# Performance work log

Measured on AMD Instinct MI355X. Metric: run time of the kernel, lower is better.

Reference implementation:

```python
import jax, jax.numpy as jnp
import numpy as np

D_IN = 2048
NUM_HEADS = 16
QK_NOPE = 64
QK_ROPE = 64
QK_HEAD = QK_NOPE + QK_ROPE  # 128
V_HEAD = 128
KV_LORA = 1024
SEQ = 4096
BATCH = 1
SCALE = QK_HEAD ** -0.5
EPS = 1e-6


def rmsnorm(x, w):
    return x * jax.lax.rsqrt(jnp.mean(x * x, axis=-1, keepdims=True) + EPS) * w


def apply_rope(x, cos, sin):
    # x: [B, S, H, D]; cos/sin: [S, D//2]; pairs are consecutive elements (view_as_complex)
    b, s, h, d = x.shape
    xr = x.reshape(b, s, h, d // 2, 2)
    xe, xo = xr[..., 0], xr[..., 1]
    c = cos[None, :, None, :]
    sn = sin[None, :, None, :]
    oe = xe * c - xo * sn
    oo = xe * sn + xo * c
    return jnp.stack([oe, oo], axis=-1).reshape(b, s, h, d)


def setup_inputs() -> dict:
    key = jax.random.key(0)
    ks = jax.random.split(key, 8)
    x = jax.random.normal(ks[0], (BATCH, SEQ, D_IN), dtype=jnp.float32)
    # rotary tables (rope_theta=10000)
    inv_freq = 1.0 / (10000.0 ** (np.arange(0, QK_ROPE, 2, dtype=np.float32) / QK_ROPE))
    angles = np.arange(SEQ, dtype=np.float32)[:, None] * inv_freq[None, :]
    cos = jnp.asarray(np.cos(angles), dtype=jnp.float32)
    sin = jnp.asarray(np.sin(angles), dtype=jnp.float32)
    # causal additive mask [S, S]
    mask = jnp.where(jnp.triu(jnp.ones((SEQ, SEQ), dtype=bool), k=1), -1e9, 0.0).astype(jnp.float32)
    def lin(k, fan_out, fan_in):
        bound = 1.0 / np.sqrt(fan_in)
        return jax.random.uniform(k, (fan_out, fan_in), jnp.float32, -bound, bound)
    wq = lin(ks[1], NUM_HEADS * QK_HEAD, D_IN)
    wkv_a = lin(ks[2], KV_LORA + QK_ROPE, D_IN)
    kv_norm_w = jnp.ones((KV_LORA,), dtype=jnp.float32)
    wkv_b = lin(ks[3], NUM_HEADS * (QK_NOPE + V_HEAD), KV_LORA)
    wo = lin(ks[4], D_IN, NUM_HEADS * V_HEAD)
    return {"x": x, "cos": cos, "sin": sin, "mask": mask, "wq": wq,
            "wkv_a": wkv_a, "kv_norm_w": kv_norm_w, "wkv_b": wkv_b, "wo": wo,
            "start_pos": 0}


def reference(x, cos, sin, mask, wq, wkv_a, kv_norm_w, wkv_b, wo, start_pos):
    b, s, _ = x.shape
    # Q projection -> [B, S, H, qk_head_dim]
    q = (x @ wq.T).reshape(b, s, NUM_HEADS, QK_HEAD)
    q_nope, q_pe = q[..., :QK_NOPE], q[..., QK_NOPE:]
    q_pe = apply_rope(q_pe, cos, sin)
    # KV low-rank projection
    kv_full = x @ wkv_a.T                               # [B, S, KV_LORA + QK_ROPE]
    kv, k_pe = kv_full[..., :KV_LORA], kv_full[..., KV_LORA:]
    k_pe = apply_rope(k_pe[:, :, None, :], cos, sin)    # [B, S, 1, QK_ROPE]
    # naive path: expand latent to per-head k_nope / v
    q = jnp.concatenate([q_nope, q_pe], axis=-1)        # [B, S, H, 128]
    kvb = (rmsnorm(kv, kv_norm_w) @ wkv_b.T).reshape(b, s, NUM_HEADS, QK_NOPE + V_HEAD)
    k_nope, v = kvb[..., :QK_NOPE], kvb[..., QK_NOPE:]
    k = jnp.concatenate([k_nope, jnp.broadcast_to(k_pe, (b, s, NUM_HEADS, QK_ROPE))], axis=-1)
    # start_pos=0 prefill: cache[:, :end_pos] == freshly written k, v
    scores = jnp.einsum('bqhd,bkhd->bqhk', q, k) * SCALE  # [B, S, H, S]
    scores = scores + mask[None, :, None, :]
    probs = jax.nn.softmax(scores.astype(jnp.float32), axis=-1).astype(x.dtype)
    out = jnp.einsum('bqhk,bkhd->bqhd', probs, v)       # [B, S, H, V_HEAD]
    return out.reshape(b, s, NUM_HEADS * V_HEAD) @ wo.T
```

## Files before the change

kernel.cpp:

```cpp
#include <hip/hip_runtime.h>

typedef __bf16 bf16;
typedef __attribute__((ext_vector_type(8))) __bf16 bf16x8;
typedef __attribute__((ext_vector_type(2))) __bf16 bf16x2;
typedef __attribute__((ext_vector_type(4))) float f32x4;
typedef __attribute__((ext_vector_type(4))) int int4v;

typedef __attribute__((address_space(1))) const void gconst_t;
typedef __attribute__((address_space(3))) void lvoid_t;

#define SEQ 4096
#define D_IN 2048
#define NHEADS 16
#define QSCALE (0.08838834764831843f * 1.4426950408889634f)
#define RMS_EPS 1e-6f

__device__ inline unsigned pack2bf(float a, float b) {
    bf16x2 t; t[0] = (bf16)a; t[1] = (bf16)b;
    return __builtin_bit_cast(unsigned, t);
}

__global__ __launch_bounds__(256) void f32_to_bf16_kernel(
    const float* __restrict__ in, bf16* __restrict__ out, int n) {
    int i = (blockIdx.x * 256 + threadIdx.x) * 4;
    int stride = gridDim.x * 256 * 4;
    for (; i < n; i += stride) {
        float4 v = *reinterpret_cast<const float4*>(in + i);
        bf16 o[4];
        o[0] = (bf16)v.x; o[1] = (bf16)v.y; o[2] = (bf16)v.z; o[3] = (bf16)v.w;
        *reinterpret_cast<uint2*>(out + i) = *reinterpret_cast<uint2*>(o);
    }
}

template<bool BF16_OUT>
__global__ __launch_bounds__(256) void gemm_bt_kernel(
    const bf16* __restrict__ A, const bf16* __restrict__ B, void* __restrict__ Cout,
    int M, int N, int K) {
    __shared__ __align__(16) bf16 Al[128 * 32];
    __shared__ __align__(16) bf16 Bl[128 * 32];
    int tid  = threadIdx.x;
    int lane = tid & 63;
    int w    = tid >> 6;
    int wr = w >> 1, wc = w & 1;
    int m0 = blockIdx.y * 128;
    int n0 = blockIdx.x * 128;
    int l15 = lane & 15;
    int g   = lane >> 4;

    int srow = (lane >> 2);
    int scol = (lane & 3) * 8;

    f32x4 acc[4][4] = {};

    for (int k0 = 0; k0 < K; k0 += 32) {
        __syncthreads();
        #pragma unroll
        for (int c = 0; c < 2; c++) {
            int arow = m0 + c*64 + w*16 + srow;
            const bf16* ga = A + (size_t)arow * K + k0 + scol;
            __builtin_amdgcn_global_load_lds((gconst_t*)ga, (lvoid_t*)&Al[c*2048 + w*512], 16, 0, 0);
            int brow = n0 + c*64 + w*16 + srow; if (brow >= N) brow = N - 1;
            const bf16* gb = B + (size_t)brow * K + k0 + scol;
            __builtin_amdgcn_global_load_lds((gconst_t*)gb, (lvoid_t*)&Bl[c*2048 + w*512], 16, 0, 0);
        }
        __syncthreads();
        bf16x8 af[4], bfv[4];
        #pragma unroll
        for (int mt = 0; mt < 4; mt++)
            af[mt] = *reinterpret_cast<const bf16x8*>(&Al[(wr*64 + mt*16 + l15) * 32 + g*8]);
        #pragma unroll
        for (int nt = 0; nt < 4; nt++)
            bfv[nt] = *reinterpret_cast<const bf16x8*>(&Bl[(wc*64 + nt*16 + l15) * 32 + g*8]);
        #pragma unroll
        for (int mt = 0; mt < 4; mt++)
            #pragma unroll
            for (int nt = 0; nt < 4; nt++)
                acc[mt][nt] = __builtin_amdgcn_mfma_f32_16x16x32_bf16(af[mt], bfv[nt], acc[mt][nt], 0, 0, 0);
    }

    #pragma unroll
    for (int mt = 0; mt < 4; mt++) {
        #pragma unroll
        for (int nt = 0; nt < 4; nt++) {
            int col = n0 + wc*64 + nt*16 + l15;
            if (col < N) {
                #pragma unroll
                for (int r = 0; r < 4; r++) {
                    int row = m0 + wr*64 + mt*16 + g*4 + r;
                    if (BF16_OUT)
                        ((bf16*)Cout)[(size_t)row * N + col] = (bf16)acc[mt][nt][r];
                    else
                        ((float*)Cout)[(size_t)row * N + col] = acc[mt][nt][r];
                }
            }
        }
    }
}

__global__ __launch_bounds__(256) void prep_q_kernel(
    bf16* __restrict__ q, const float* __restrict__ cosb, const float* __restrict__ sinb) {
    int s = blockIdx.x;
    int t = threadIdx.x;
    bf16* p = q + (size_t)s * 2048 + t * 8;
    bf16x8 v = *reinterpret_cast<bf16x8*>(p);
    float f[8];
    #pragma unroll
    for (int j = 0; j < 8; j++) f[j] = (float)v[j];
    int d0 = (t & 15) * 8;
    if (d0 >= 64) {
        int ib = (d0 - 64) >> 1;
        #pragma unroll
        for (int pr = 0; pr < 4; pr++) {
            float c  = cosb[s * 32 + ib + pr];
            float sn = sinb[s * 32 + ib + pr];
            float xe = f[pr*2], xo = f[pr*2 + 1];
            f[pr*2]     = xe * c - xo * sn;
            f[pr*2 + 1] = xe * sn + xo * c;
        }
    }
    #pragma unroll
    for (int j = 0; j < 8; j++) v[j] = (bf16)(f[j] * QSCALE);
    *reinterpret_cast<bf16x8*>(p) = v;
}

__global__ __launch_bounds__(256) void prep_kv_kernel(
    const bf16* __restrict__ kvfull, const float* __restrict__ w,
    const float* __restrict__ cosb, const float* __restrict__ sinb,
    bf16* __restrict__ kvnorm, bf16* __restrict__ kpe) {
    __shared__ float red[4];
    int s = blockIdx.x;
    int t = threadIdx.x;
    const bf16* src = kvfull + (size_t)s * 1088;
    float f[4];
    {
        uint2 raw = *reinterpret_cast<const uint2*>(src + t * 4);
        bf16* vb = reinterpret_cast<bf16*>(&raw);
        float ss = 0.f;
        #pragma unroll
        for (int j = 0; j < 4; j++) { f[j] = (float)vb[j]; ss += f[j] * f[j]; }
        #pragma unroll
        for (int m = 1; m < 64; m <<= 1) ss += __shfl_xor(ss, m);
        if ((t & 63) == 0) red[t >> 6] = ss;
    }
    __syncthreads();
    float tot = red[0] + red[1] + red[2] + red[3];
    float rms = rsqrtf(tot * (1.0f / 1024.0f) + RMS_EPS);
    bf16 o[4];
    #pragma unroll
    for (int j = 0; j < 4; j++) o[j] = (bf16)(f[j] * rms * w[t*4 + j]);
    *reinterpret_cast<uint2*>(kvnorm + (size_t)s * 1024 + t * 4) = *reinterpret_cast<uint2*>(o);
    if (t < 16) {
        float e[4];
        #pragma unroll
        for (int j = 0; j < 4; j++) e[j] = (float)src[1024 + t*4 + j];
        int ib = t * 2;
        float c0 = cosb[s*32 + ib],     s0 = sinb[s*32 + ib];
        float c1 = cosb[s*32 + ib + 1], s1 = sinb[s*32 + ib + 1];
        bf16 ko[4];
        ko[0] = (bf16)(e[0]*c0 - e[1]*s0);
        ko[1] = (bf16)(e[0]*s0 + e[1]*c0);
        ko[2] = (bf16)(e[2]*c1 - e[3]*s1);
        ko[3] = (bf16)(e[2]*s1 + e[3]*c1);
        *reinterpret_cast<uint2*>(kpe + (size_t)s * 64 + t * 4) = *reinterpret_cast<uint2*>(ko);
    }
}

__global__ __launch_bounds__(256) void build_vt_kernel(
    const bf16* __restrict__ kvb, bf16* __restrict__ vt) {
    const int LT = 130;
    __shared__ bf16 lt[64 * 130];
    int h  = blockIdx.y;
    int s0 = blockIdx.x * 64;
    int t  = threadIdx.x;
    {
        int row = t >> 2;
        int d0  = (t & 3) * 32;
        const bf16* src = kvb + (size_t)(s0 + row) * 3072 + h * 192 + 64 + d0;
        int4v v0 = *reinterpret_cast<const int4v*>(src);
        int4v v1 = *reinterpret_cast<const int4v*>(src + 8);
        int4v v2 = *reinterpret_cast<const int4v*>(src + 16);
        int4v v3 = *reinterpret_cast<const int4v*>(src + 24);
        int* dst = reinterpret_cast<int*>(&lt[row * LT + d0]);
        int* s0p = reinterpret_cast<int*>(&v0); int* s1p = reinterpret_cast<int*>(&v1);
        int* s2p = reinterpret_cast<int*>(&v2); int* s3p = reinterpret_cast<int*>(&v3);
        #pragma unroll
        for (int j = 0; j < 4; j++) { dst[j] = s0p[j]; dst[4+j] = s1p[j]; dst[8+j] = s2p[j]; dst[12+j] = s3p[j]; }
    }
    __syncthreads();
    int ss = t & 63;
    int db = t >> 6;
    bf16* out = vt + (size_t)h * 128 * 4096 + s0 + ss;
    #pragma unroll
    for (int dd = db; dd < 128; dd += 4)
        out[(size_t)dd * 4096] = lt[ss * LT + dd];
}

__global__ __launch_bounds__(256, 2) void attn_kernel(
    const bf16* __restrict__ q,
    const bf16* __restrict__ kvb,
    const bf16* __restrict__ kpe,
    const bf16* __restrict__ vt,
    bf16* __restrict__ attn) {
    const int LPS = 72;
    __shared__ __align__(16) bf16 Kl[2][64 * 128];
    __shared__ __align__(16) bf16 Vl[2][128 * 64];
    __shared__ __align__(16) bf16 Pl[4][16 * 72];
    __shared__ __align__(16) float bcast[4][16];

    int h    = blockIdx.y;
    int tile = (h < 8) ? (31 - (int)blockIdx.x) : (int)blockIdx.x;
    int q0   = tile * 128;
    int t  = threadIdx.x;
    int lane = t & 63;
    int w  = t >> 6;
    int l15 = lane & 15;
    int g   = lane >> 4;
    int sw  = l15 & 7;
    int qrow = q0 + w * 32;

    const bf16* kvbh = kvb + h * 192;
    const bf16* vth  = vt + (size_t)h * 524288;

    bf16x8 qf[2][4];
    #pragma unroll
    for (int mt = 0; mt < 2; mt++) {
        const bf16* qp = q + (size_t)(qrow + mt*16 + l15) * 2048 + h * 128 + g * 8;
        #pragma unroll
        for (int c = 0; c < 4; c++) qf[mt][c] = *reinterpret_cast<const bf16x8*>(qp + c * 32);
    }

    f32x4 o[2][8] = {};
    float mrow[2], lrow[2];
    #pragma unroll
    for (int mt = 0; mt < 2; mt++) { mrow[mt] = -3e38f; lrow[mt] = 0.f; }

    int nch = (q0 >> 6) + 2;
    int dc  = (q0 >> 6) + (w >> 1);

    auto stageK = [&](int jc, int buf) {
        int j0 = jc << 6;
        #pragma unroll
        for (int c = 0; c < 4; c++) {
            int idx = c*256 + w*64 + lane;
            int row = idx >> 4;
            int u   = (idx & 15) ^ (row & 7);
            const bf16* src = (u < 8)
                ? kvbh + (size_t)(j0 + row) * 3072 + u * 8
                : kpe  + (size_t)(j0 + row) * 64  + (u - 8) * 8;
            __builtin_amdgcn_global_load_lds((gconst_t*)src,
                (lvoid_t*)&Kl[buf][(c*256 + w*64) * 8], 16, 0, 0);
        }
    };
    auto stageV = [&](int jc, int buf) {
        int j0 = jc << 6;
        #pragma unroll
        for (int c = 0; c < 4; c++) {
            int idx = c*256 + w*64 + lane;
            int row = idx >> 3;
            int u   = (idx & 7) ^ (row & 7);
            const bf16* src = vth + (size_t)row * 4096 + j0 + u * 8;
            __builtin_amdgcn_global_load_lds((gconst_t*)src,
                (lvoid_t*)&Vl[buf][(c*256 + w*64) * 8], 16, 0, 0);
        }
    };

    stageK(0, 0); stageV(0, 0);

    for (int jc = 0; jc < nch; ++jc) {
        __syncthreads();
        if (jc + 1 < nch) { stageK(jc + 1, (jc + 1) & 1); stageV(jc + 1, (jc + 1) & 1); }

        if (jc <= dc) {
            int cur = jc & 1;
            int j0  = jc << 6;
            bool masked = (jc == dc);

            f32x4 sfr[2][4];
            #pragma unroll
            for (int s = 0; s < 4; ++s) {
                int krow = s*16 + l15;
                bf16x8 kf[4];
                #pragma unroll
                for (int c = 0; c < 4; ++c)
                    kf[c] = *reinterpret_cast<const bf16x8*>(
                        &Kl[cur][krow*128 + (((c*4 + g) ^ sw) * 8)]);
                #pragma unroll
                for (int mt = 0; mt < 2; ++mt) {
                    f32x4 acc = {};
                    acc = __builtin_amdgcn_mfma_f32_16x16x32_bf16(kf[0], qf[mt][0], acc, 0, 0, 0);
                    acc = __builtin_amdgcn_mfma_f32_16x16x32_bf16(kf[1], qf[mt][1], acc, 0, 0, 0);
                    acc = __builtin_amdgcn_mfma_f32_16x16x32_bf16(kf[2], qf[mt][2], acc, 0, 0, 0);
                    acc = __builtin_amdgcn_mfma_f32_16x16x32_bf16(kf[3], qf[mt][3], acc, 0, 0, 0);
                    sfr[mt][s] = acc;
                }
            }

            bf16x8 pf[2][2];
            #pragma unroll
            for (int mt = 0; mt < 2; ++mt) {
                int i = qrow + mt*16 + l15;
                if (masked) {
                    #pragma unroll
                    for (int s = 0; s < 4; ++s)
                        #pragma unroll
                        for (int r = 0; r < 4; ++r) {
                            int j = j0 + s*16 + g*4 + r;
                            if (j > i) sfr[mt][s][r] = -3e38f;
                        }
                }
                float m01 = fmaxf(fmaxf(sfr[mt][0][0], sfr[mt][0][1]),
                                  fmaxf(sfr[mt][0][2], sfr[mt][0][3]));
                float m23 = fmaxf(fmaxf(sfr[mt][1][0], sfr[mt][1][1]),
                                  fmaxf(sfr[mt][1][2], sfr[mt][1][3]));
                float m45 = fmaxf(fmaxf(sfr[mt][2][0], sfr[mt][2][1]),
                                  fmaxf(sfr[mt][2][2], sfr[mt][2][3]));
                float m67 = fmaxf(fmaxf(sfr[mt][3][0], sfr[mt][3][1]),
                                  fmaxf(sfr[mt][3][2], sfr[mt][3][3]));
                float mloc = fmaxf(fmaxf(m01, m23), fmaxf(m45, m67));
                float mx = fmaxf(mloc, __shfl_xor(mloc, 16));
                mx = fmaxf(mx, __shfl_xor(mx, 32));
                bool need = mx > mrow[mt];
                float mnew = fmaxf(mrow[mt], mx);
                float sfac = __builtin_amdgcn_exp2f(mrow[mt] - mnew);
                mrow[mt] = mnew;
                float psum = 0.f;
                #pragma unroll
                for (int s = 0; s < 4; ++s)
                    #pragma unroll
                    for (int r = 0; r < 4; ++r) {
                        float p = __builtin_amdgcn_exp2f(sfr[mt][s][r] - mnew);
                        sfr[mt][s][r] = p;
                        psum += p;
                    }
                lrow[mt] = lrow[mt] * sfac + psum;
                #pragma unroll
                for (int s = 0; s < 4; ++s) {
                    unsigned u0 = pack2bf(sfr[mt][s][0], sfr[mt][s][1]);
                    unsigned u1 = pack2bf(sfr[mt][s][2], sfr[mt][s][3]);
                    *reinterpret_cast<unsigned*>(&Pl[w][l15 * LPS + s*16 + g*4])     = u0;
                    *reinterpret_cast<unsigned*>(&Pl[w][l15 * LPS + s*16 + g*4 + 2]) = u1;
                }
                if (g == 0) bcast[w][l15] = sfac;
                f32x4 sf4 = *reinterpret_cast<const f32x4*>(&bcast[w][g*4]);
                if (__any(need)) {
                    #pragma unroll
                    for (int dt = 0; dt < 8; ++dt)
                        #pragma unroll
                        for (int r = 0; r < 4; ++r) o[mt][dt][r] *= sf4[r];
                }
                pf[mt][0] = *reinterpret_cast<const bf16x8*>(&Pl[w][l15 * LPS + g * 8]);
                pf[mt][1] = *reinterpret_cast<const bf16x8*>(&Pl[w][l15 * LPS + 32 + g * 8]);
            }

            #pragma unroll
            for (int dt = 0; dt < 8; ++dt) {
                int vrow = dt*16 + l15;
                bf16x8 va = *reinterpret_cast<const bf16x8*>(
                    &Vl[cur][vrow*64 + ((g ^ sw) * 8)]);
                bf16x8 vb = *reinterpret_cast<const bf16x8*>(
                    &Vl[cur][vrow*64 + (((4 + g) ^ sw) * 8)]);
                o[0][dt] = __builtin_amdgcn_mfma_f32_16x16x32_bf16(pf[0][0], va, o[0][dt], 0, 0, 0);
                o[0][dt] = __builtin_amdgcn_mfma_f32_16x16x32_bf16(pf[0][1], vb, o[0][dt], 0, 0, 0);
                o[1][dt] = __builtin_amdgcn_mfma_f32_16x16x32_bf16(pf[1][0], va, o[1][dt], 0, 0, 0);
                o[1][dt] = __builtin_amdgcn_mfma_f32_16x16x32_bf16(pf[1][1], vb, o[1][dt], 0, 0, 0);
            }
        }
    }

    #pragma unroll
    for (int mt = 0; mt < 2; ++mt) {
        float l = lrow[mt];
        l += __shfl_xor(l, 16);
        l += __shfl_xor(l, 32);
        float linv = __builtin_amdgcn_rcpf(l);
        if (g == 0) bcast[w][l15] = linv;
        f32x4 li4 = *reinterpret_cast<const f32x4*>(&bcast[w][g*4]);
        #pragma unroll
        for (int r = 0; r < 4; ++r) {
            int i = qrow + mt*16 + g*4 + r;
            #pragma unroll
            for (int dt = 0; dt < 8; ++dt)
                attn[(size_t)i * 2048 + h * 128 + dt*16 + l15] = (bf16)(o[mt][dt][r] * li4[r]);
        }
    }
}

extern "C" void kernel_launch(void* const* d_in, const int* in_sizes, int n_in,
                              void* d_out, int out_size, void* d_ws, size_t ws_size,
                              hipStream_t stream) {
    const float* x    = (const float*)d_in[0];
    const float* cosb = (const float*)d_in[1];
    const float* sinb = (const float*)d_in[2];
    const float* wq   = (const float*)d_in[4];
    const float* wkva = (const float*)d_in[5];
    const float* kvw  = (const float*)d_in[6];
    const float* wkvb = (const float*)d_in[7];
    const float* wo   = (const float*)d_in[8];

    char* ws = (char*)d_ws;
    bf16* x_bf    = (bf16*)(ws + 0);
    bf16* kvnorm  = (bf16*)(ws + 0);
    bf16* attn    = (bf16*)(ws + 0);
    bf16* wq_bf   = (bf16*)(ws + 16777216);
    bf16* wkva_bf = (bf16*)(ws + 25165824);
    bf16* wkvb_bf = (bf16*)(ws + 29622272);
    bf16* wo_bf   = (bf16*)(ws + 35913728);
    bf16* q_bf    = (bf16*)(ws + 44302336);
    bf16* kvfull  = (bf16*)(ws + 61079552);
    bf16* kpe     = (bf16*)(ws + 69992448);
    bf16* kvb     = (bf16*)(ws + 70516736);
    bf16* vt      = (bf16*)(ws + 95682560);

    f32_to_bf16_kernel<<<dim3(512), dim3(256), 0, stream>>>(x,    x_bf,    4096*2048);
    f32_to_bf16_kernel<<<dim3(512), dim3(256), 0, stream>>>(wq,   wq_bf,   2048*2048);
    f32_to_bf16_kernel<<<dim3(512), dim3(256), 0, stream>>>(wkva, wkva_bf, 1088*2048);
    f32_to_bf16_kernel<<<dim3(512), dim3(256), 0, stream>>>(wkvb, wkvb_bf, 3072*1024);
    f32_to_bf16_kernel<<<dim3(512), dim3(256), 0, stream>>>(wo,   wo_bf,   2048*2048);

    gemm_bt_kernel<true><<<dim3(16, 32), dim3(256), 0, stream>>>(x_bf, wq_bf,   q_bf,   4096, 2048, 2048);
    gemm_bt_kernel<true><<<dim3(9,  32), dim3(256), 0, stream>>>(x_bf, wkva_bf, kvfull, 4096, 1088, 2048);

    prep_q_kernel <<<dim3(4096), dim3(256), 0, stream>>>(q_bf, cosb, sinb);
    prep_kv_kernel<<<dim3(4096), dim3(256), 0, stream>>>(kvfull, kvw, cosb, sinb, kvnorm, kpe);

    gemm_bt_kernel<true><<<dim3(24, 32), dim3(256), 0, stream>>>(kvnorm, wkvb_bf, kvb, 4096, 3072, 1024);

    build_vt_kernel<<<dim3(64, 16), dim3(256), 0, stream>>>(kvb, vt);

    attn_kernel<<<dim3(32, 16), dim3(256), 0, stream>>>(q_bf, kvb, kpe, vt, attn);

    gemm_bt_kernel<false><<<dim3(16, 32), dim3(256), 0, stream>>>(attn, wo_bf, (float*)d_out, 4096, 2048, 2048);
}
```

Measured before the change: 382.7 us.

## Fuse Q and KV-A projections into one GEMM, merge conversions, raise MFMA priority

The Q and KV-A weight buffers sit back to back in the workspace, so one GEMM with N=3136 now writes a combined qkv buffer. The prep kernels and attention read Q and KV from that buffer with the new row stride. The five fp32-to-bf16 conversion launches are merged into one kernel. s_setprio is raised around the QK and PV MFMA loops in attention. The aim is to cut launch overhead and GEMM tail waste, in exchange for a strided Q layout in the attention loads.

```diff
diff --git a/kernel.cpp b/kernel.cpp
--- a/kernel.cpp
+++ b/kernel.cpp
@@ -14,22 +14,36 @@
 #define NHEADS 16
 #define QSCALE (0.08838834764831843f * 1.4426950408889634f)
 #define RMS_EPS 1e-6f
+#define QKV_N 3136
 
 __device__ inline unsigned pack2bf(float a, float b) {
     bf16x2 t; t[0] = (bf16)a; t[1] = (bf16)b;
     return __builtin_bit_cast(unsigned, t);
 }
 
-__global__ __launch_bounds__(256) void f32_to_bf16_kernel(
-    const float* __restrict__ in, bf16* __restrict__ out, int n) {
-    int i = (blockIdx.x * 256 + threadIdx.x) * 4;
-    int stride = gridDim.x * 256 * 4;
-    for (; i < n; i += stride) {
+__device__ inline void conv_seg(const float* __restrict__ in, bf16* __restrict__ out,
+                                int n, int i0, int stride) {
+    for (int i = i0; i < n; i += stride) {
         float4 v = *reinterpret_cast<const float4*>(in + i);
         bf16 o[4];
         o[0] = (bf16)v.x; o[1] = (bf16)v.y; o[2] = (bf16)v.z; o[3] = (bf16)v.w;
         *reinterpret_cast<uint2*>(out + i) = *reinterpret_cast<uint2*>(o);
     }
+}
+
+__global__ __launch_bounds__(256) void convert_all_kernel(
+    const float* __restrict__ xs,  const float* __restrict__ wqs,
+    const float* __restrict__ was, const float* __restrict__ wbs,
+    const float* __restrict__ wos,
+    bf16* __restrict__ xd, bf16* __restrict__ wqd, bf16* __restrict__ wad,
+    bf16* __restrict__ wbd, bf16* __restrict__ wod) {
+    int i0 = (blockIdx.x * 256 + threadIdx.x) * 4;
+    int stride = gridDim.x * 256 * 4;
+    conv_seg(xs,  xd,  4096 * 2048, i0, stride);
+    conv_seg(wqs, wqd, 2048 * 2048, i0, stride);
+    conv_seg(was, wad, 1088 * 2048, i0, stride);
+    conv_seg(wbs, wbd, 3072 * 1024, i0, stride);
+    conv_seg(wos, wod, 2048 * 2048, i0, stride);
 }
 
 template<bool BF16_OUT>
@@ -98,10 +112,10 @@
 }
 
 __global__ __launch_bounds__(256) void prep_q_kernel(
-    bf16* __restrict__ q, const float* __restrict__ cosb, const float* __restrict__ sinb) {
+    bf16* __restrict__ qkv, const float* __restrict__ cosb, const float* __restrict__ sinb) {
     int s = blockIdx.x;
     int t = threadIdx.x;
-    bf16* p = q + (size_t)s * 2048 + t * 8;
+    bf16* p = qkv + (size_t)s * QKV_N + t * 8;
     bf16x8 v = *reinterpret_cast<bf16x8*>(p);
     float f[8];
     #pragma unroll
@@ -124,13 +138,13 @@
 }
 
 __global__ __launch_bounds__(256) void prep_kv_kernel(
-    const bf16* __restrict__ kvfull, const float* __restrict__ w,
+    const bf16* __restrict__ qkv, const float* __restrict__ w,
     const float* __restrict__ cosb, const float* __restrict__ sinb,
     bf16* __restrict__ kvnorm, bf16* __restrict__ kpe) {
     __shared__ float red[4];
     int s = blockIdx.x;
     int t = threadIdx.x;
-    const bf16* src = kvfull + (size_t)s * 1088;
+    const bf16* src = qkv + (size_t)s * QKV_N + 2048;
     float f[4];
     {
         uint2 raw = *reinterpret_cast<const uint2*>(src + t * 4);
@@ -224,7 +238,7 @@
     bf16x8 qf[2][4];
     #pragma unroll
     for (int mt = 0; mt < 2; mt++) {
-        const bf16* qp = q + (size_t)(qrow + mt*16 + l15) * 2048 + h * 128 + g * 8;
+        const bf16* qp = q + (size_t)(qrow + mt*16 + l15) * QKV_N + h * 128 + g * 8;
         #pragma unroll
         for (int c = 0; c < 4; c++) qf[mt][c] = *reinterpret_cast<const bf16x8*>(qp + c * 32);
     }
@@ -276,6 +290,7 @@
             bool masked = (jc == dc);
 
             f32x4 sfr[2][4];
+            __builtin_amdgcn_s_setprio(1);
             #pragma unroll
             for (int s = 0; s < 4; ++s) {
                 int krow = s*16 + l15;
@@ -294,6 +309,7 @@
                     sfr[mt][s] = acc;
                 }
             }
+            __builtin_amdgcn_s_setprio(0);
 
             bf16x8 pf[2][2];
             #pragma unroll
@@ -352,6 +368,7 @@
                 pf[mt][1] = *reinterpret_cast<const bf16x8*>(&Pl[w][l15 * LPS + 32 + g * 8]);
             }
 
+            __builtin_amdgcn_s_setprio(1);
             #pragma unroll
             for (int dt = 0; dt < 8; ++dt) {
                 int vrow = dt*16 + l15;
@@ -364,6 +381,7 @@
                 o[1][dt] = __builtin_amdgcn_mfma_f32_16x16x32_bf16(pf[1][0], va, o[1][dt], 0, 0, 0);
                 o[1][dt] = __builtin_amdgcn_mfma_f32_16x16x32_bf16(pf[1][1], vb, o[1][dt], 0, 0, 0);
             }
+            __builtin_amdgcn_s_setprio(0);
         }
     }
 
@@ -405,29 +423,24 @@
     bf16* wkva_bf = (bf16*)(ws + 25165824);
     bf16* wkvb_bf = (bf16*)(ws + 29622272);
     bf16* wo_bf   = (bf16*)(ws + 35913728);
-    bf16* q_bf    = (bf16*)(ws + 44302336);
-    bf16* kvfull  = (bf16*)(ws + 61079552);
+    bf16* qkv     = (bf16*)(ws + 44302336);
     bf16* kpe     = (bf16*)(ws + 69992448);
     bf16* kvb     = (bf16*)(ws + 70516736);
     bf16* vt      = (bf16*)(ws + 95682560);
 
-    f32_to_bf16_kernel<<<dim3(512), dim3(256), 0, stream>>>(x,    x_bf,    4096*2048);
-    f32_to_bf16_kernel<<<dim3(512), dim3(256), 0, stream>>>(wq,   wq_bf,   2048*2048);
-    f32_to_bf16_kernel<<<dim3(512), dim3(256), 0, stream>>>(wkva, wkva_bf, 1088*2048);
-    f32_to_bf16_kernel<<<dim3(512), dim3(256), 0, stream>>>(wkvb, wkvb_bf, 3072*1024);
-    f32_to_bf16_kernel<<<dim3(512), dim3(256), 0, stream>>>(wo,   wo_bf,   2048*2048);
-
-    gemm_bt_kernel<true><<<dim3(16, 32), dim3(256), 0, stream>>>(x_bf, wq_bf,   q_bf,   4096, 2048, 2048);
-    gemm_bt_kernel<true><<<dim3(9,  32), dim3(256), 0, stream>>>(x_bf, wkva_bf, kvfull, 4096, 1088, 2048);
-
-    prep_q_kernel <<<dim3(4096), dim3(256), 0, stream>>>(q_bf, cosb, sinb);
-    prep_kv_kernel<<<dim3(4096), dim3(256), 0, stream>>>(kvfull, kvw, cosb, sinb, kvnorm, kpe);
+    convert_all_kernel<<<dim3(2048), dim3(256), 0, stream>>>(
+        x, wq, wkva, wkvb, wo, x_bf, wq_bf, wkva_bf, wkvb_bf, wo_bf);
+
+    gemm_bt_kernel<true><<<dim3(25, 32), dim3(256), 0, stream>>>(x_bf, wq_bf, qkv, 4096, QKV_N, 2048);
+
+    prep_q_kernel <<<dim3(4096), dim3(256), 0, stream>>>(qkv, cosb, sinb);
+    prep_kv_kernel<<<dim3(4096), dim3(256), 0, stream>>>(qkv, kvw, cosb, sinb, kvnorm, kpe);
 
     gemm_bt_kernel<true><<<dim3(24, 32), dim3(256), 0, stream>>>(kvnorm, wkvb_bf, kvb, 4096, 3072, 1024);
 
     build_vt_kernel<<<dim3(64, 16), dim3(256), 0, stream>>>(kvb, vt);
 
-    attn_kernel<<<dim3(32, 16), dim3(256), 0, stream>>>(q_bf, kvb, kpe, vt, attn);
+    attn_kernel<<<dim3(32, 16), dim3(256), 0, stream>>>(qkv, kvb, kpe, vt, attn);
 
     gemm_bt_kernel<false><<<dim3(16, 32), dim3(256), 0, stream>>>(attn, wo_bf, (float*)d_out, 4096, 2048, 2048);
 }
```

New measurement: 373.5 us. -2.4%, faster.
